# Kernel tuning notes

Hardware: AMD Instinct MI355X
Metric: run time of the kernel (lower is better)

Reference implementation:

```python
import jax, jax.numpy as jnp
import numpy as np

D = 1024  # input_dim

def setup_inputs() -> dict:
    key = jax.random.key(0)
    ks = jax.random.split(key, 8)
    x = jax.random.normal(ks[0], (8, 2048, D), dtype=jnp.float32)
    q = jax.random.normal(ks[1], (8, 1024, D), dtype=jnp.float32)
    s = 1.0 / np.sqrt(D)
    Wq = jax.random.normal(ks[2], (D, D), dtype=jnp.float32) * s
    bq = jnp.zeros((D,), dtype=jnp.float32)
    Wk = jax.random.normal(ks[3], (D, D), dtype=jnp.float32) * s
    bk = jnp.zeros((D,), dtype=jnp.float32)
    Wv = jax.random.normal(ks[4], (D, D), dtype=jnp.float32) * s
    bv = jnp.zeros((D,), dtype=jnp.float32)
    return {"x": x, "q": q, "Wq": Wq, "bq": bq, "Wk": Wk, "bk": bk, "Wv": Wv, "bv": bv}

def reference(x, q, Wq, bq, Wk, bk, Wv, bv):
    # Linear layers: y = in @ W^T + b (torch nn.Linear convention)
    queries = jnp.einsum('bqd,ed->bqe', q, Wq) + bq   # [B, Lq, D]
    keys    = jnp.einsum('bkd,ed->bke', x, Wk) + bk   # [B, Lk, D]
    values  = jnp.einsum('bkd,ed->bke', x, Wv) + bv   # [B, Lk, D]
    scale = 1.0 / jnp.sqrt(jnp.asarray(D, dtype=queries.dtype))
    scores = jnp.einsum('bqd,bkd->bqk', queries, keys) * scale  # [B, Lq, Lk]
    attention = jax.nn.softmax(scores, axis=2)
    weighted = jnp.einsum('bqk,bkd->bqd', attention, values)    # [B, Lq, D]
    return (weighted, jnp.squeeze(attention, axis=1) if attention.shape[1] == 1 else attention)
```

## Files before the change

### kernel.cpp

```cpp
#include <hip/hip_runtime.h>
#include <hip/hip_bf16.h>

typedef __attribute__((ext_vector_type(8))) short short8;
typedef __attribute__((ext_vector_type(4))) short short4v;
typedef __attribute__((ext_vector_type(4))) float f32x4;
using u16 = unsigned short;

__device__ __forceinline__ u16 f2bf(float x) {
    __hip_bfloat16 h = __float2bfloat16(x);
    return *reinterpret_cast<u16*>(&h);
}

__device__ __forceinline__ void async16(void* lds, const void* g) {
    __builtin_amdgcn_global_load_lds((__attribute__((address_space(1))) void*)g,
                                     (__attribute__((address_space(3))) void*)lds,
                                     16, 0, 0);
}

__global__ __launch_bounds__(256)
void f32_to_bf16_kernel(const float* __restrict__ in, u16* __restrict__ out, long n) {
    long i = ((long)blockIdx.x * 256 + threadIdx.x) * 8;
    if (i + 8 > n) return;
    float4 a = *(const float4*)(in + i);
    float4 b = *(const float4*)(in + i + 4);
    short8 p;
    p[0] = (short)f2bf(a.x); p[1] = (short)f2bf(a.y);
    p[2] = (short)f2bf(a.z); p[3] = (short)f2bf(a.w);
    p[4] = (short)f2bf(b.x); p[5] = (short)f2bf(b.y);
    p[6] = (short)f2bf(b.z); p[7] = (short)f2bf(b.w);
    *(short8*)(out + i) = p;
}

template<bool A_F32, bool OUT_BF16, bool ADD_BIAS, bool TRANS_C>
__global__ __launch_bounds__(256, 2)
void gemm_bt_kernel(const void* __restrict__ Av, const u16* __restrict__ B,
                    void* __restrict__ Cv, const float* __restrict__ bias,
                    float scale, int M, int N, int K,
                    long Abatch, long Bbatch, long Cbatch)
{
    __shared__ u16 As[128 * 32];
    __shared__ u16 Bs[128 * 32];

    const int tid  = threadIdx.x;
    const int wid  = tid >> 6;
    const int lane = tid & 63;

    B += (long)blockIdx.z * Bbatch;

    const int bm = blockIdx.y * 128;
    const int bn = blockIdx.x * 128;

    const int wr = (wid >> 1) * 64;
    const int wc = (wid & 1) * 64;

    f32x4 acc[4][4] = {};

    const int srow = tid >> 2;
    const int scol = (tid & 3) * 8;
    const u16*   aptrb = nullptr;
    const float* aptrf = nullptr;
    if constexpr (A_F32) {
        aptrf = (const float*)Av + (long)blockIdx.z * Abatch
                + (long)(bm + srow) * K + scol;
    } else {
        aptrb = (const u16*)Av + (long)blockIdx.z * Abatch
                + (long)(bm + srow) * K + scol;
    }
    const u16* bptr = B + (long)(bn + srow) * K + scol;
    char* asb = (char*)As + wid * 1024;
    char* bsb = (char*)Bs + wid * 1024;

    const int lr = lane & 15;
    const int lk = (lane >> 4) * 8;

    const int nk = K >> 5;
    for (int kt = 0; kt < nk; ++kt) {
        const u16* bk = bptr + kt * 32;
        async16(bsb,        bk);
        async16(bsb + 4096, bk + (long)64 * K);
        if constexpr (A_F32) {
            const float* a0 = aptrf + kt * 32;
            float4 u0 = *(const float4*)a0;
            float4 u1 = *(const float4*)(a0 + 4);
            float4 w0 = *(const float4*)(a0 + (long)64 * K);
            float4 w1 = *(const float4*)(a0 + (long)64 * K + 4);
            short8 s0, s1;
            s0[0] = (short)f2bf(u0.x); s0[1] = (short)f2bf(u0.y);
            s0[2] = (short)f2bf(u0.z); s0[3] = (short)f2bf(u0.w);
            s0[4] = (short)f2bf(u1.x); s0[5] = (short)f2bf(u1.y);
            s0[6] = (short)f2bf(u1.z); s0[7] = (short)f2bf(u1.w);
            s1[0] = (short)f2bf(w0.x); s1[1] = (short)f2bf(w0.y);
            s1[2] = (short)f2bf(w0.z); s1[3] = (short)f2bf(w0.w);
            s1[4] = (short)f2bf(w1.x); s1[5] = (short)f2bf(w1.y);
            s1[6] = (short)f2bf(w1.z); s1[7] = (short)f2bf(w1.w);
            *(short8*)((char*)As + tid * 16)        = s0;
            *(short8*)((char*)As + 4096 + tid * 16) = s1;
        } else {
            const u16* ak = aptrb + kt * 32;
            async16(asb,        ak);
            async16(asb + 4096, ak + (long)64 * K);
        }
        __syncthreads();

        short8 af[4], bfr[4];
        #pragma unroll
        for (int i = 0; i < 4; ++i)
            af[i] = *(const short8*)&As[(wr + i * 16 + lr) * 32 + lk];
        #pragma unroll
        for (int j = 0; j < 4; ++j)
            bfr[j] = *(const short8*)&Bs[(wc + j * 16 + lr) * 32 + lk];

        #pragma unroll
        for (int i = 0; i < 4; ++i)
            #pragma unroll
            for (int j = 0; j < 4; ++j)
                acc[i][j] = __builtin_amdgcn_mfma_f32_16x16x32_bf16(
                                af[i], bfr[j], acc[i][j], 0, 0, 0);
        __syncthreads();
    }

    const int r0 = (lane >> 4) * 4;
    const long crow = bm + wr + r0;
    const long ccol = bn + wc + lr;
    if constexpr (TRANS_C) {
        u16* C = (u16*)Cv;
        #pragma unroll
        for (int i = 0; i < 4; ++i) {
            const long row = crow + i * 16;
            const long zb = row >> 11, rr = row & 2047;
            #pragma unroll
            for (int j = 0; j < 4; ++j) {
                float bb = 0.f;
                if constexpr (ADD_BIAS) bb = bias[ccol + j * 16];
                short4v pk;
                #pragma unroll
                for (int r = 0; r < 4; ++r)
                    pk[r] = (short)f2bf(acc[i][j][r] * scale + bb);
                *(short4v*)(C + zb * 2097152 + (ccol + j * 16) * 2048 + rr) = pk;
            }
        }
    } else if constexpr (OUT_BF16) {
        u16* C = (u16*)Cv + (long)blockIdx.z * Cbatch;
        #pragma unroll
        for (int i = 0; i < 4; ++i)
            #pragma unroll
            for (int j = 0; j < 4; ++j) {
                float bb = 0.f;
                if constexpr (ADD_BIAS) bb = bias[ccol + j * 16];
                #pragma unroll
                for (int r = 0; r < 4; ++r)
                    C[(crow + i * 16 + r) * (long)N + ccol + j * 16] =
                        f2bf(acc[i][j][r] * scale + bb);
            }
    } else {
        float* C = (float*)Cv + (long)blockIdx.z * Cbatch;
        #pragma unroll
        for (int i = 0; i < 4; ++i)
            #pragma unroll
            for (int j = 0; j < 4; ++j) {
                float bb = 0.f;
                if constexpr (ADD_BIAS) bb = bias[ccol + j * 16];
                #pragma unroll
                for (int r = 0; r < 4; ++r)
                    C[(crow + i * 16 + r) * (long)N + ccol + j * 16] =
                        acc[i][j][r] * scale + bb;
            }
    }
}

__global__ __launch_bounds__(256)
void softmax_kernel(float* __restrict__ S, int L) {
    const long base = (long)blockIdx.x * L;
    float* row = S + base;
    const int t = threadIdx.x;
    const int lane = t & 63, wid = t >> 6;

    float4 v0 = ((const float4*)row)[2 * t];
    float4 v1 = ((const float4*)row)[2 * t + 1];

    float m = fmaxf(fmaxf(fmaxf(v0.x, v0.y), fmaxf(v0.z, v0.w)),
                    fmaxf(fmaxf(v1.x, v1.y), fmaxf(v1.z, v1.w)));
    #pragma unroll
    for (int off = 32; off; off >>= 1) m = fmaxf(m, __shfl_xor(m, off));

    __shared__ float red[8];
    if (lane == 0) red[wid] = m;
    __syncthreads();
    m = fmaxf(fmaxf(red[0], red[1]), fmaxf(red[2], red[3]));

    v0.x = __expf(v0.x - m); v0.y = __expf(v0.y - m);
    v0.z = __expf(v0.z - m); v0.w = __expf(v0.w - m);
    v1.x = __expf(v1.x - m); v1.y = __expf(v1.y - m);
    v1.z = __expf(v1.z - m); v1.w = __expf(v1.w - m);

    float s = ((v0.x + v0.y) + (v0.z + v0.w)) + ((v1.x + v1.y) + (v1.z + v1.w));
    #pragma unroll
    for (int off = 32; off; off >>= 1) s += __shfl_xor(s, off);
    if (lane == 0) red[4 + wid] = s;
    __syncthreads();
    s = (red[4] + red[5]) + (red[6] + red[7]);

    const float inv = 1.0f / s;
    v0.x *= inv; v0.y *= inv; v0.z *= inv; v0.w *= inv;
    v1.x *= inv; v1.y *= inv; v1.z *= inv; v1.w *= inv;

    ((float4*)row)[2 * t]     = v0;
    ((float4*)row)[2 * t + 1] = v1;
}

extern "C" void kernel_launch(void* const* d_in, const int* in_sizes, int n_in,
                              void* d_out, int out_size, void* d_ws, size_t ws_size,
                              hipStream_t stream) {
    const float* x  = (const float*)d_in[0];
    const float* q  = (const float*)d_in[1];
    const float* Wq = (const float*)d_in[2];
    const float* bq = (const float*)d_in[3];
    const float* Wk = (const float*)d_in[4];
    const float* bk = (const float*)d_in[5];
    const float* Wv = (const float*)d_in[6];
    const float* bv = (const float*)d_in[7];
    float* out = (float*)d_out;

    u16* ws  = (u16*)d_ws;
    u16* wqb = ws;
    u16* wkb = ws + 1048576;
    u16* wvb = ws + 2097152;
    u16* Qbf = ws + 3145728;
    u16* Kbf = ws + 11534336;
    u16* Vt  = ws + 3145728;

    float* Sout = out + 8388608;

    dim3 blk(256);

    f32_to_bf16_kernel<<<512, blk, 0, stream>>>(Wq, wqb, 1048576L);
    f32_to_bf16_kernel<<<512, blk, 0, stream>>>(Wk, wkb, 1048576L);
    f32_to_bf16_kernel<<<512, blk, 0, stream>>>(Wv, wvb, 1048576L);

    gemm_bt_kernel<true, true, true, false><<<dim3(8, 64, 1), blk, 0, stream>>>(
        q, wqb, Qbf, bq, 1.0f, 8192, 1024, 1024, 0, 0, 0);

    gemm_bt_kernel<true, true, true, false><<<dim3(8, 128, 1), blk, 0, stream>>>(
        x, wkb, Kbf, bk, 1.0f, 16384, 1024, 1024, 0, 0, 0);

    gemm_bt_kernel<false, false, false, false><<<dim3(16, 8, 8), blk, 0, stream>>>(
        Qbf, Kbf, Sout, nullptr, 0.03125f, 1024, 2048, 1024,
        1048576, 2097152, 2097152);

    softmax_kernel<<<8192, blk, 0, stream>>>(Sout, 2048);

    gemm_bt_kernel<true, true, true, true><<<dim3(8, 128, 1), blk, 0, stream>>>(
        x, wvb, Vt, bv, 1.0f, 16384, 1024, 1024, 0, 0, 0);

    gemm_bt_kernel<true, false, false, false><<<dim3(8, 8, 8), blk, 0, stream>>>(
        Sout, Vt, out, nullptr, 1.0f, 1024, 1024, 2048,
        2097152, 2097152, 1048576);
}
```

Baseline: 514.0 us.

## Fuse K and V projections into one GEMM and add XCD-aware block remapping

```diff
diff --git a/kernel.cpp b/kernel.cpp
--- a/kernel.cpp
+++ b/kernel.cpp
@@ -31,24 +31,40 @@
     *(short8*)(out + i) = p;
 }
 
-template<bool A_F32, bool OUT_BF16, bool ADD_BIAS, bool TRANS_C>
+template<bool A_F32, bool OUT_BF16, bool ADD_BIAS, bool KV_FUSED>
 __global__ __launch_bounds__(256, 2)
 void gemm_bt_kernel(const void* __restrict__ Av, const u16* __restrict__ B,
-                    void* __restrict__ Cv, const float* __restrict__ bias,
+                    void* __restrict__ Cv, u16* __restrict__ C2,
+                    const float* __restrict__ bias, const float* __restrict__ bias2,
                     float scale, int M, int N, int K,
                     long Abatch, long Bbatch, long Cbatch)
 {
     __shared__ u16 As[128 * 32];
     __shared__ u16 Bs[128 * 32];
 
+    int bx = blockIdx.x, by = blockIdx.y, bz = blockIdx.z;
+    {
+        const int gx = gridDim.x, gy = gridDim.y;
+        const int nwg = gx * gy * gridDim.z;
+        if ((nwg & 7) == 0) {
+            const int b = bx + gx * (by + gy * bz);
+            const int cpx = nwg >> 3;
+            const int s = (b & 7) * cpx + (b >> 3);
+            bx = s % gx;
+            const int t = s / gx;
+            by = t % gy;
+            bz = t / gy;
+        }
+    }
+
     const int tid  = threadIdx.x;
     const int wid  = tid >> 6;
     const int lane = tid & 63;
 
-    B += (long)blockIdx.z * Bbatch;
-
-    const int bm = blockIdx.y * 128;
-    const int bn = blockIdx.x * 128;
+    B += (long)bz * Bbatch;
+
+    const int bm = by * 128;
+    const int bn = bx * 128;
 
     const int wr = (wid >> 1) * 64;
     const int wc = (wid & 1) * 64;
@@ -60,11 +76,9 @@
     const u16*   aptrb = nullptr;
     const float* aptrf = nullptr;
     if constexpr (A_F32) {
-        aptrf = (const float*)Av + (long)blockIdx.z * Abatch
-                + (long)(bm + srow) * K + scol;
+        aptrf = (const float*)Av + (long)bz * Abatch + (long)(bm + srow) * K + scol;
     } else {
-        aptrb = (const u16*)Av + (long)blockIdx.z * Abatch
-                + (long)(bm + srow) * K + scol;
+        aptrb = (const u16*)Av + (long)bz * Abatch + (long)(bm + srow) * K + scol;
     }
     const u16* bptr = B + (long)(bn + srow) * K + scol;
     char* asb = (char*)As + wid * 1024;
@@ -122,25 +136,38 @@
     const int r0 = (lane >> 4) * 4;
     const long crow = bm + wr + r0;
     const long ccol = bn + wc + lr;
-    if constexpr (TRANS_C) {
-        u16* C = (u16*)Cv;
-        #pragma unroll
-        for (int i = 0; i < 4; ++i) {
-            const long row = crow + i * 16;
-            const long zb = row >> 11, rr = row & 2047;
-            #pragma unroll
-            for (int j = 0; j < 4; ++j) {
-                float bb = 0.f;
-                if constexpr (ADD_BIAS) bb = bias[ccol + j * 16];
-                short4v pk;
-                #pragma unroll
-                for (int r = 0; r < 4; ++r)
-                    pk[r] = (short)f2bf(acc[i][j][r] * scale + bb);
-                *(short4v*)(C + zb * 2097152 + (ccol + j * 16) * 2048 + rr) = pk;
+    if constexpr (KV_FUSED) {
+        if (bn < 1024) {
+            u16* C = (u16*)Cv;
+            #pragma unroll
+            for (int i = 0; i < 4; ++i)
+                #pragma unroll
+                for (int j = 0; j < 4; ++j) {
+                    const float bb = bias[ccol + j * 16];
+                    #pragma unroll
+                    for (int r = 0; r < 4; ++r)
+                        C[(crow + i * 16 + r) * 1024L + ccol + j * 16] =
+                            f2bf(acc[i][j][r] + bb);
+                }
+        } else {
+            #pragma unroll
+            for (int i = 0; i < 4; ++i) {
+                const long row = crow + i * 16;
+                const long zb = row >> 11, rr = row & 2047;
+                #pragma unroll
+                for (int j = 0; j < 4; ++j) {
+                    const long feat = ccol - 1024 + j * 16;
+                    const float bb = bias2[feat];
+                    short4v pk;
+                    #pragma unroll
+                    for (int r = 0; r < 4; ++r)
+                        pk[r] = (short)f2bf(acc[i][j][r] + bb);
+                    *(short4v*)(C2 + zb * 2097152 + feat * 2048 + rr) = pk;
+                }
             }
         }
     } else if constexpr (OUT_BF16) {
-        u16* C = (u16*)Cv + (long)blockIdx.z * Cbatch;
+        u16* C = (u16*)Cv + (long)bz * Cbatch;
         #pragma unroll
         for (int i = 0; i < 4; ++i)
             #pragma unroll
@@ -153,7 +180,7 @@
                         f2bf(acc[i][j][r] * scale + bb);
             }
     } else {
-        float* C = (float*)Cv + (long)blockIdx.z * Cbatch;
+        float* C = (float*)Cv + (long)bz * Cbatch;
         #pragma unroll
         for (int i = 0; i < 4; ++i)
             #pragma unroll
@@ -227,7 +254,7 @@
     u16* wvb = ws + 2097152;
     u16* Qbf = ws + 3145728;
     u16* Kbf = ws + 11534336;
-    u16* Vt  = ws + 3145728;
+    u16* Vt  = ws + 28311552;
 
     float* Sout = out + 8388608;
 
@@ -238,21 +265,18 @@
     f32_to_bf16_kernel<<<512, blk, 0, stream>>>(Wv, wvb, 1048576L);
 
     gemm_bt_kernel<true, true, true, false><<<dim3(8, 64, 1), blk, 0, stream>>>(
-        q, wqb, Qbf, bq, 1.0f, 8192, 1024, 1024, 0, 0, 0);
-
-    gemm_bt_kernel<true, true, true, false><<<dim3(8, 128, 1), blk, 0, stream>>>(
-        x, wkb, Kbf, bk, 1.0f, 16384, 1024, 1024, 0, 0, 0);
+        q, wqb, Qbf, nullptr, bq, nullptr, 1.0f, 8192, 1024, 1024, 0, 0, 0);
+
+    gemm_bt_kernel<true, true, true, true><<<dim3(16, 128, 1), blk, 0, stream>>>(
+        x, wkb, Kbf, Vt, bk, bv, 1.0f, 16384, 2048, 1024, 0, 0, 0);
 
     gemm_bt_kernel<false, false, false, false><<<dim3(16, 8, 8), blk, 0, stream>>>(
-        Qbf, Kbf, Sout, nullptr, 0.03125f, 1024, 2048, 1024,
+        Qbf, Kbf, Sout, nullptr, nullptr, nullptr, 0.03125f, 1024, 2048, 1024,
         1048576, 2097152, 2097152);
 
     softmax_kernel<<<8192, blk, 0, stream>>>(Sout, 2048);
 
-    gemm_bt_kernel<true, true, true, true><<<dim3(8, 128, 1), blk, 0, stream>>>(
-        x, wvb, Vt, bv, 1.0f, 16384, 1024, 1024, 0, 0, 0);
-
     gemm_bt_kernel<true, false, false, false><<<dim3(8, 8, 8), blk, 0, stream>>>(
-        Sout, Vt, out, nullptr, 1.0f, 1024, 1024, 2048,
+        Sout, Vt, out, nullptr, nullptr, nullptr, 1.0f, 1024, 1024, 2048,
         2097152, 2097152, 1048576);
 }
```

Result: faster. 446.6 us (-13.1%).
